# Kernel tuning notes

Measured on AMD Instinct MI355X. Metric: run time of the kernel, lower is better.

## Reference

```python
import jax, jax.numpy as jnp
import numpy as np
import math

B, T, J, D = 16, 243, 24, 256
H, W = 8, 4  # num_heads, half-window


def setup_inputs() -> dict:
    key = jax.random.key(0)
    k1, k2 = jax.random.split(key, 2)
    x_tan_seq = jax.random.normal(k1, (B, T, J, D), dtype=jnp.float32)
    W_qkv = jax.random.normal(k2, (3 * D, D), dtype=jnp.float32) * 0.02
    b_qkv = jnp.zeros((3 * D,), dtype=jnp.float32)
    tau = jnp.ones((H,), dtype=jnp.float32)
    return {"x_tan_seq": x_tan_seq, "W_qkv": W_qkv, "b_qkv": b_qkv, "tau": tau}


def reference(x_tan_seq, W_qkv, b_qkv, tau):
    Bb, Tt, Jj, Dd = x_tan_seq.shape
    d_h = Dd // H
    KW = 2 * W + 1
    # [B,T,J,D] -> [B*J, T, D]
    x = x_tan_seq.transpose(0, 2, 1, 3).reshape(Bb * Jj, Tt, Dd)
    # fused qkv projection (torch Linear: x @ W.T + b)
    qkv = x @ W_qkv.T + b_qkv                      # [BJ, T, 3D]
    qkv = qkv.reshape(Bb * Jj, Tt, 3, H, d_h)
    q = qkv[:, :, 0].transpose(0, 2, 1, 3)          # [BJ, H, T, dh]
    k = qkv[:, :, 1].transpose(0, 2, 1, 3)
    v = qkv[:, :, 2].transpose(0, 2, 1, 3)
    # replicate-pad time axis, then gather sliding windows
    k_pad = jnp.pad(k, ((0, 0), (0, 0), (W, W), (0, 0)), mode='edge')
    v_pad = jnp.pad(v, ((0, 0), (0, 0), (W, W), (0, 0)), mode='edge')
    idx = jnp.arange(Tt)[:, None] + jnp.arange(KW)[None, :]  # [T, KW] into padded axis
    k_win = k_pad[:, :, idx, :]                    # [BJ, H, T, KW, dh]
    v_win = v_pad[:, :, idx, :]
    tau_c = jnp.clip(tau, 0.001)[None, :, None, None]  # clamp(min=0.001)
    logits = jnp.einsum('bhtd,bhtkd->bhtk', q, k_win) / (math.sqrt(d_h) * tau_c)
    # mask out-of-bounds (replicated) frames
    frame = jnp.arange(Tt)[:, None] + (jnp.arange(KW)[None, :] - W)
    oob = (frame < 0) | (frame >= Tt)              # [T, KW]
    logits = jnp.where(oob[None, None], -jnp.inf, logits)
    attn = jax.nn.softmax(logits, axis=-1)
    agg = jnp.einsum('bhtk,bhtkd->bhtd', attn, v_win)  # [BJ, H, T, dh]
    out = agg.transpose(0, 2, 1, 3).reshape(Bb, Jj, Tt, Dd).transpose(0, 2, 1, 3)
    return out  # [B, T, J, D]
```

## Files before the change

### kernel.cpp

```cpp
#include <hip/hip_runtime.h>
#include <hip/hip_bf16.h>
#include <math.h>

typedef __hip_bfloat16 bf16;
typedef __attribute__((ext_vector_type(8))) short short8;
typedef __attribute__((ext_vector_type(4))) float float4v;

#define Tsz 243
#define Jsz 24
#define Dsz 256
#define Hsz 8
#define Wsz 4
#define KWsz 9
#define SEQ 384
#define Ksz 256
#define JDsz 6144
#define MB 128
#define T0B 122

#define XN_ELEMS 23887872
#define XN4 5971968
#define WN4 49152
#define TOT4 (XN4 + WN4)

#define LDST 72
#define KOFFs 5120
#define VTOFFs 10240
#define VTSTR 136
#define POFFs 16128
#define PSTR 72
#define SMEM_SHORTS (POFFs + 8 * 16 * PSTR)
#define SMEM_BYTES (SMEM_SHORTS * 2)

__device__ __forceinline__ bool tau_is_fp32(const void* tau) {
    return *(const unsigned int*)tau == 0x3F800000u;
}

__device__ __forceinline__ unsigned int pack2(float a, float b) {
    const unsigned int lo = (unsigned int)__builtin_bit_cast(unsigned short, __float2bfloat16(a));
    const unsigned int hi = (unsigned int)__builtin_bit_cast(unsigned short, __float2bfloat16(b));
    return lo | (hi << 16);
}
__device__ __forceinline__ unsigned short bf16bits(float x) {
    return __builtin_bit_cast(unsigned short, __float2bfloat16(x));
}

__global__ __launch_bounds__(256, 4)
void conv_prepass(const void* __restrict__ xp, const void* __restrict__ Wp,
                  const void* __restrict__ taup, unsigned int* __restrict__ ws)
{
    if (!tau_is_fp32(taup)) return;
    const float4* xf = (const float4*)xp;
    const float4* wf = (const float4*)Wp;
    const int stride = (int)gridDim.x * 256;
    for (int i = (int)blockIdx.x * 256 + (int)threadIdx.x; i < TOT4; i += stride) {
        const float4 v = (i < XN4) ? xf[i] : wf[i - XN4];
        ((uint2*)ws)[i] = make_uint2(pack2(v.x, v.y), pack2(v.z, v.w));
    }
}

__global__ __launch_bounds__(512, 6)
void fused_qkv_attn(const void* __restrict__ xp, const void* __restrict__ Wp,
                    const void* __restrict__ bp, const void* __restrict__ taup,
                    const bf16* __restrict__ wsb, void* __restrict__ out)
{
    __shared__ __align__(16) bf16 smem[SMEM_SHORTS];
    bf16* As = smem;
    bf16* Bs = smem + 128 * LDST;
    unsigned short* s16 = (unsigned short*)smem;

    const bool is32 = tau_is_fp32(taup);
    const bf16* xAll = is32 ? wsb : (const bf16*)xp;
    const bf16* wAll = is32 ? (wsb + XN_ELEMS) : (const bf16*)Wp;

    const int bid     = (int)blockIdx.x;
    const int logical = (bid & 7) * (SEQ * Hsz * 2 / 8) + (bid >> 3);
    const int s    = logical >> 4;
    const int h    = (logical >> 1) & 7;
    const int blk2 = logical & 1;
    const int b = s / Jsz;
    const int j = s - b * Jsz;
    const int r0 = blk2 ? (Tsz - MB) : 0;

    const int tid  = (int)threadIdx.x;
    const int wave = tid >> 6;
    const int lane = tid & 63;
    const int fr = lane & 15;
    const int fk = (lane >> 4) * 8;
    const int wm32 = (wave >> 1) * 32;
    const int wn   = (wave & 1) * 48;

    const int arow = tid >> 2;
    const int acol = (tid & 3) << 4;
    const bf16* xw = xAll + ((size_t)(b * Tsz + r0 + arow) * Jsz + j) * (size_t)Dsz + acol;
    bf16* aDst = As + arow * LDST + acol;

    const int brow = tid >> 2;
    const int bcol = (tid & 3) << 4;
    const int wrow = ((brow >> 5) << 8) + (h << 5) + (brow & 31);
    const bf16* ww = wAll + (size_t)wrow * Ksz + bcol;
    bf16* bDst = Bs + brow * LDST + bcol;

    float4v acc[2][3];
#pragma unroll
    for (int i = 0; i < 2; ++i)
#pragma unroll
        for (int n = 0; n < 3; ++n)
            acc[i][n] = (float4v){0.f, 0.f, 0.f, 0.f};

    for (int kt = 0; kt < Ksz; kt += 64) {
        {
            const uint4 a0 = *(const uint4*)(xw + kt);
            const uint4 a1 = *(const uint4*)(xw + kt + 8);
            *(uint4*)aDst       = a0;
            *(uint4*)(aDst + 8) = a1;
            if (tid < 384) {
                const uint4 b0 = *(const uint4*)(ww + kt);
                const uint4 b1 = *(const uint4*)(ww + kt + 8);
                *(uint4*)bDst       = b0;
                *(uint4*)(bDst + 8) = b1;
            }
        }
        __syncthreads();
#pragma unroll
        for (int ks = 0; ks < 2; ++ks) {
            short8 af[2], bfr[3];
#pragma unroll
            for (int i = 0; i < 2; ++i)
                af[i] = *(const short8*)(As + (wm32 + (i << 4) + fr) * LDST + (ks << 5) + fk);
#pragma unroll
            for (int n = 0; n < 3; ++n)
                bfr[n] = *(const short8*)(Bs + (wn + (n << 4) + fr) * LDST + (ks << 5) + fk);
#pragma unroll
            for (int i = 0; i < 2; ++i)
#pragma unroll
                for (int n = 0; n < 3; ++n)
                    acc[i][n] = __builtin_amdgcn_mfma_f32_16x16x32_bf16(af[i], bfr[n], acc[i][n], 0, 0, 0);
        }
        __syncthreads();
    }

    const int r0acc = (lane >> 4) << 2;
    if ((wave & 1) == 0) {
        const float b0 = is32 ? ((const float*)bp)[(h << 5) + fr]        : __bfloat162float(((const bf16*)bp)[(h << 5) + fr]);
        const float b1 = is32 ? ((const float*)bp)[(h << 5) + 16 + fr]   : __bfloat162float(((const bf16*)bp)[(h << 5) + 16 + fr]);
        const float b2 = is32 ? ((const float*)bp)[256 + (h << 5) + fr]  : __bfloat162float(((const bf16*)bp)[256 + (h << 5) + fr]);
#pragma unroll
        for (int i = 0; i < 2; ++i) {
            const int tb = wm32 + (i << 4) + r0acc;
#pragma unroll
            for (int r = 0; r < 4; ++r) {
                const int t = tb + r;
                s16[t * 40 + fr]              = bf16bits(acc[i][0][r] + b0);
                s16[t * 40 + 16 + fr]         = bf16bits(acc[i][1][r] + b1);
                s16[KOFFs + t * 40 + fr]      = bf16bits(acc[i][2][r] + b2);
            }
        }
    } else {
        const float b0 = is32 ? ((const float*)bp)[256 + (h << 5) + 16 + fr] : __bfloat162float(((const bf16*)bp)[256 + (h << 5) + 16 + fr]);
        const float b1 = is32 ? ((const float*)bp)[512 + (h << 5) + fr]      : __bfloat162float(((const bf16*)bp)[512 + (h << 5) + fr]);
        const float b2 = is32 ? ((const float*)bp)[512 + (h << 5) + 16 + fr] : __bfloat162float(((const bf16*)bp)[512 + (h << 5) + 16 + fr]);
#pragma unroll
        for (int i = 0; i < 2; ++i) {
            const int tb = wm32 + (i << 4) + r0acc;
#pragma unroll
            for (int r = 0; r < 4; ++r) {
                const int t = tb + r;
                s16[KOFFs + t * 40 + 16 + fr]        = bf16bits(acc[i][0][r] + b0);
                s16[VTOFFs + fr * VTSTR + t]         = bf16bits(acc[i][1][r] + b1);
                s16[VTOFFs + (16 + fr) * VTSTR + t]  = bf16bits(acc[i][2][r] + b2);
            }
        }
    }
    __syncthreads();

    const float tv = is32 ? ((const float*)taup)[h]
                          : __bfloat162float(((const bf16*)taup)[h]);
    const float scale = 1.0f / (5.656854249f * fmaxf(tv, 0.001f));
    const int g  = wave;
    const int wb = (g <= 1) ? 0 : ((g >= 5) ? 64 : ((g - 1) << 4));

    const short8 qf = *(const short8*)((const bf16*)s16 + (g * 16 + fr) * 40 + fk);
    float4v sacc[4];
#pragma unroll
    for (int s2 = 0; s2 < 4; ++s2) {
        const short8 kf = *(const short8*)((const bf16*)s16 + KOFFs + (wb + s2 * 16 + fr) * 40 + fk);
        sacc[s2] = __builtin_amdgcn_mfma_f32_16x16x32_bf16(qf, kf, (float4v){0.f,0.f,0.f,0.f}, 0, 0, 0);
    }

    float vv[4][4];
    const int dly = (lane & 15) + wb - (g << 4) - r0acc;
#pragma unroll
    for (int s2 = 0; s2 < 4; ++s2)
#pragma unroll
        for (int r = 0; r < 4; ++r) {
            const int dd = dly + s2 * 16 - r;
            vv[s2][r] = ((unsigned)(dd + 4) <= 8u) ? sacc[s2][r] * scale : -1e30f;
        }

    float inv[4];
#pragma unroll
    for (int r = 0; r < 4; ++r) {
        float m = fmaxf(fmaxf(vv[0][r], vv[1][r]), fmaxf(vv[2][r], vv[3][r]));
        m = fmaxf(m, __shfl_xor(m, 1, 64));
        m = fmaxf(m, __shfl_xor(m, 2, 64));
        m = fmaxf(m, __shfl_xor(m, 4, 64));
        m = fmaxf(m, __shfl_xor(m, 8, 64));
        float dsum = 0.f;
#pragma unroll
        for (int s2 = 0; s2 < 4; ++s2) {
            vv[s2][r] = __expf(vv[s2][r] - m);
            dsum += vv[s2][r];
        }
        dsum += __shfl_xor(dsum, 1, 64);
        dsum += __shfl_xor(dsum, 2, 64);
        dsum += __shfl_xor(dsum, 4, 64);
        dsum += __shfl_xor(dsum, 8, 64);
        inv[r] = 1.0f / fmaxf(dsum, 1e-30f);
    }

    unsigned short* pb = s16 + POFFs + g * (16 * PSTR);
#pragma unroll
    for (int s2 = 0; s2 < 4; ++s2)
#pragma unroll
        for (int r = 0; r < 4; ++r)
            pb[(r0acc + r) * PSTR + s2 * 16 + (lane & 15)] = bf16bits(vv[s2][r] * inv[r]);

    float4v oacc[2] = {(float4v){0.f,0.f,0.f,0.f}, (float4v){0.f,0.f,0.f,0.f}};
#pragma unroll
    for (int ks = 0; ks < 2; ++ks) {
        const short8 pa = *(const short8*)((const bf16*)pb + fr * PSTR + ks * 32 + fk);
#pragma unroll
        for (int nt = 0; nt < 2; ++nt) {
            const short8 vb = *(const short8*)((const bf16*)s16 + VTOFFs +
                                               (nt * 16 + fr) * VTSTR + wb + ks * 32 + fk);
            oacc[nt] = __builtin_amdgcn_mfma_f32_16x16x32_bf16(pa, vb, oacc[nt], 0, 0, 0);
        }
    }

#pragma unroll
    for (int r = 0; r < 4; ++r) {
        const int tl   = (g << 4) + r0acc + r;
        const int tOut = r0 + tl;
        const bool own = blk2 ? (tOut >= T0B) : (tOut < T0B);
        if (own) {
            const size_t obase = ((size_t)(b * Tsz + tOut) * Jsz + j) * (size_t)Dsz
                               + (h << 5) + (lane & 15);
            if (is32) {
                ((float*)out)[obase]      = oacc[0][r];
                ((float*)out)[obase + 16] = oacc[1][r];
            } else {
                ((bf16*)out)[obase]      = __float2bfloat16(oacc[0][r]);
                ((bf16*)out)[obase + 16] = __float2bfloat16(oacc[1][r]);
            }
        }
    }
}

extern "C" void kernel_launch(void* const* d_in, const int* in_sizes, int n_in,
                              void* d_out, int out_size, void* d_ws, size_t ws_size,
                              hipStream_t stream) {
    (void)in_sizes; (void)n_in; (void)out_size; (void)ws_size;
    conv_prepass<<<2048, 256, 0, stream>>>(d_in[0], d_in[1], d_in[3], (unsigned int*)d_ws);
    fused_qkv_attn<<<SEQ * Hsz * 2, 512, 0, stream>>>(d_in[0], d_in[1], d_in[2], d_in[3],
                                                      (const bf16*)d_ws, d_out);
}
```

Baseline: 255.0 us.

## Transpose x to sequence-major in prepass and shrink attention window tiles

The prepass now writes x into [B,J,T,D] order, so the fused kernel's A-tile loads read contiguous rows instead of rows strided by J*D. The attention stage now uses a 32-key window per 16-query group instead of 64, which halves the QK and PV MFMAs, the softmax work and the P buffer size. The prepass also runs in the bf16 path and uses twice as many blocks. The cost is the index divisions in the prepass and scattered writes to the workspace.

```diff
diff --git a/kernel.cpp b/kernel.cpp
--- a/kernel.cpp
+++ b/kernel.cpp
@@ -11,26 +11,21 @@
 #define Dsz 256
 #define Hsz 8
 #define Wsz 4
-#define KWsz 9
 #define SEQ 384
 #define Ksz 256
-#define JDsz 6144
 #define MB 128
 #define T0B 122
 
 #define XN_ELEMS 23887872
-#define XN4 5971968
-#define WN4 49152
-#define TOT4 (XN4 + WN4)
+#define XU2 5971968
+#define WU2 49152
 
 #define LDST 72
 #define KOFFs 5120
 #define VTOFFs 10240
 #define VTSTR 136
 #define POFFs 16128
-#define PSTR 72
-#define SMEM_SHORTS (POFFs + 8 * 16 * PSTR)
-#define SMEM_BYTES (SMEM_SHORTS * 2)
+#define SMEM_SHORTS (POFFs + 8 * 16 * 40)
 
 __device__ __forceinline__ bool tau_is_fp32(const void* tau) {
     return *(const unsigned int*)tau == 0x3F800000u;
@@ -47,21 +42,38 @@
 
 __global__ __launch_bounds__(256, 4)
 void conv_prepass(const void* __restrict__ xp, const void* __restrict__ Wp,
-                  const void* __restrict__ taup, unsigned int* __restrict__ ws)
+                  const void* __restrict__ taup, uint2* __restrict__ ws)
 {
-    if (!tau_is_fp32(taup)) return;
-    const float4* xf = (const float4*)xp;
-    const float4* wf = (const float4*)Wp;
+    const bool is32 = tau_is_fp32(taup);
     const int stride = (int)gridDim.x * 256;
-    for (int i = (int)blockIdx.x * 256 + (int)threadIdx.x; i < TOT4; i += stride) {
-        const float4 v = (i < XN4) ? xf[i] : wf[i - XN4];
-        ((uint2*)ws)[i] = make_uint2(pack2(v.x, v.y), pack2(v.z, v.w));
+    const int tid0 = (int)blockIdx.x * 256 + (int)threadIdx.x;
+    for (int i = tid0; i < XU2; i += stride) {
+        const int d4 = i & 63;
+        const int r  = i >> 6;
+        const int jj = r % Jsz;
+        const int r2 = r / Jsz;
+        const int t  = r2 % Tsz;
+        const int bb = r2 / Tsz;
+        const int o  = ((bb * Jsz + jj) * Tsz + t) * 64 + d4;
+        if (is32) {
+            const float4 v = ((const float4*)xp)[i];
+            ws[o] = make_uint2(pack2(v.x, v.y), pack2(v.z, v.w));
+        } else {
+            ws[o] = ((const uint2*)xp)[i];
+        }
+    }
+    for (int i = tid0; i < WU2; i += stride) {
+        if (is32) {
+            const float4 v = ((const float4*)Wp)[i];
+            ws[XU2 + i] = make_uint2(pack2(v.x, v.y), pack2(v.z, v.w));
+        } else {
+            ws[XU2 + i] = ((const uint2*)Wp)[i];
+        }
     }
 }
 
 __global__ __launch_bounds__(512, 6)
-void fused_qkv_attn(const void* __restrict__ xp, const void* __restrict__ Wp,
-                    const void* __restrict__ bp, const void* __restrict__ taup,
+void fused_qkv_attn(const void* __restrict__ bp, const void* __restrict__ taup,
                     const bf16* __restrict__ wsb, void* __restrict__ out)
 {
     __shared__ __align__(16) bf16 smem[SMEM_SHORTS];
@@ -70,8 +82,8 @@
     unsigned short* s16 = (unsigned short*)smem;
 
     const bool is32 = tau_is_fp32(taup);
-    const bf16* xAll = is32 ? wsb : (const bf16*)xp;
-    const bf16* wAll = is32 ? (wsb + XN_ELEMS) : (const bf16*)Wp;
+    const bf16* xAll = wsb;
+    const bf16* wAll = wsb + XN_ELEMS;
 
     const int bid     = (int)blockIdx.x;
     const int logical = (bid & 7) * (SEQ * Hsz * 2 / 8) + (bid >> 3);
@@ -92,7 +104,7 @@
 
     const int arow = tid >> 2;
     const int acol = (tid & 3) << 4;
-    const bf16* xw = xAll + ((size_t)(b * Tsz + r0 + arow) * Jsz + j) * (size_t)Dsz + acol;
+    const bf16* xw = xAll + ((size_t)(s * Tsz + r0 + arow)) * (size_t)Dsz + acol;
     bf16* aDst = As + arow * LDST + acol;
 
     const int brow = tid >> 2;
@@ -142,18 +154,18 @@
 
     const int r0acc = (lane >> 4) << 2;
     if ((wave & 1) == 0) {
-        const float b0 = is32 ? ((const float*)bp)[(h << 5) + fr]        : __bfloat162float(((const bf16*)bp)[(h << 5) + fr]);
-        const float b1 = is32 ? ((const float*)bp)[(h << 5) + 16 + fr]   : __bfloat162float(((const bf16*)bp)[(h << 5) + 16 + fr]);
-        const float b2 = is32 ? ((const float*)bp)[256 + (h << 5) + fr]  : __bfloat162float(((const bf16*)bp)[256 + (h << 5) + fr]);
+        const float b0 = is32 ? ((const float*)bp)[(h << 5) + fr]       : __bfloat162float(((const bf16*)bp)[(h << 5) + fr]);
+        const float b1 = is32 ? ((const float*)bp)[(h << 5) + 16 + fr]  : __bfloat162float(((const bf16*)bp)[(h << 5) + 16 + fr]);
+        const float b2 = is32 ? ((const float*)bp)[256 + (h << 5) + fr] : __bfloat162float(((const bf16*)bp)[256 + (h << 5) + fr]);
 #pragma unroll
         for (int i = 0; i < 2; ++i) {
             const int tb = wm32 + (i << 4) + r0acc;
 #pragma unroll
             for (int r = 0; r < 4; ++r) {
                 const int t = tb + r;
-                s16[t * 40 + fr]              = bf16bits(acc[i][0][r] + b0);
-                s16[t * 40 + 16 + fr]         = bf16bits(acc[i][1][r] + b1);
-                s16[KOFFs + t * 40 + fr]      = bf16bits(acc[i][2][r] + b2);
+                s16[t * 40 + fr]         = bf16bits(acc[i][0][r] + b0);
+                s16[t * 40 + 16 + fr]    = bf16bits(acc[i][1][r] + b1);
+                s16[KOFFs + t * 40 + fr] = bf16bits(acc[i][2][r] + b2);
             }
         }
     } else {
@@ -166,9 +178,9 @@
 #pragma unroll
             for (int r = 0; r < 4; ++r) {
                 const int t = tb + r;
-                s16[KOFFs + t * 40 + 16 + fr]        = bf16bits(acc[i][0][r] + b0);
-                s16[VTOFFs + fr * VTSTR + t]         = bf16bits(acc[i][1][r] + b1);
-                s16[VTOFFs + (16 + fr) * VTSTR + t]  = bf16bits(acc[i][2][r] + b2);
+                s16[KOFFs + t * 40 + 16 + fr]       = bf16bits(acc[i][0][r] + b0);
+                s16[VTOFFs + fr * VTSTR + t]        = bf16bits(acc[i][1][r] + b1);
+                s16[VTOFFs + (16 + fr) * VTSTR + t] = bf16bits(acc[i][2][r] + b2);
             }
         }
     }
@@ -177,21 +189,22 @@
     const float tv = is32 ? ((const float*)taup)[h]
                           : __bfloat162float(((const bf16*)taup)[h]);
     const float scale = 1.0f / (5.656854249f * fmaxf(tv, 0.001f));
-    const int g  = wave;
-    const int wb = (g <= 1) ? 0 : ((g >= 5) ? 64 : ((g - 1) << 4));
+    const int g = wave;
+    int wb2 = (g << 4) - 8;
+    wb2 = wb2 < 0 ? 0 : (wb2 > 96 ? 96 : wb2);
 
     const short8 qf = *(const short8*)((const bf16*)s16 + (g * 16 + fr) * 40 + fk);
-    float4v sacc[4];
-#pragma unroll
-    for (int s2 = 0; s2 < 4; ++s2) {
-        const short8 kf = *(const short8*)((const bf16*)s16 + KOFFs + (wb + s2 * 16 + fr) * 40 + fk);
+    float4v sacc[2];
+#pragma unroll
+    for (int s2 = 0; s2 < 2; ++s2) {
+        const short8 kf = *(const short8*)((const bf16*)s16 + KOFFs + (wb2 + s2 * 16 + fr) * 40 + fk);
         sacc[s2] = __builtin_amdgcn_mfma_f32_16x16x32_bf16(qf, kf, (float4v){0.f,0.f,0.f,0.f}, 0, 0, 0);
     }
 
-    float vv[4][4];
-    const int dly = (lane & 15) + wb - (g << 4) - r0acc;
-#pragma unroll
-    for (int s2 = 0; s2 < 4; ++s2)
+    float vv[2][4];
+    const int dly = (lane & 15) + wb2 - (g << 4) - r0acc;
+#pragma unroll
+    for (int s2 = 0; s2 < 2; ++s2)
 #pragma unroll
         for (int r = 0; r < 4; ++r) {
             const int dd = dly + s2 * 16 - r;
@@ -201,17 +214,14 @@
     float inv[4];
 #pragma unroll
     for (int r = 0; r < 4; ++r) {
-        float m = fmaxf(fmaxf(vv[0][r], vv[1][r]), fmaxf(vv[2][r], vv[3][r]));
+        float m = fmaxf(vv[0][r], vv[1][r]);
         m = fmaxf(m, __shfl_xor(m, 1, 64));
         m = fmaxf(m, __shfl_xor(m, 2, 64));
         m = fmaxf(m, __shfl_xor(m, 4, 64));
         m = fmaxf(m, __shfl_xor(m, 8, 64));
-        float dsum = 0.f;
-#pragma unroll
-        for (int s2 = 0; s2 < 4; ++s2) {
-            vv[s2][r] = __expf(vv[s2][r] - m);
-            dsum += vv[s2][r];
-        }
+        vv[0][r] = __expf(vv[0][r] - m);
+        vv[1][r] = __expf(vv[1][r] - m);
+        float dsum = vv[0][r] + vv[1][r];
         dsum += __shfl_xor(dsum, 1, 64);
         dsum += __shfl_xor(dsum, 2, 64);
         dsum += __shfl_xor(dsum, 4, 64);
@@ -219,23 +229,20 @@
         inv[r] = 1.0f / fmaxf(dsum, 1e-30f);
     }
 
-    unsigned short* pb = s16 + POFFs + g * (16 * PSTR);
-#pragma unroll
-    for (int s2 = 0; s2 < 4; ++s2)
+    unsigned short* pb = s16 + POFFs + g * (16 * 40);
+#pragma unroll
+    for (int s2 = 0; s2 < 2; ++s2)
 #pragma unroll
         for (int r = 0; r < 4; ++r)
-            pb[(r0acc + r) * PSTR + s2 * 16 + (lane & 15)] = bf16bits(vv[s2][r] * inv[r]);
-
-    float4v oacc[2] = {(float4v){0.f,0.f,0.f,0.f}, (float4v){0.f,0.f,0.f,0.f}};
-#pragma unroll
-    for (int ks = 0; ks < 2; ++ks) {
-        const short8 pa = *(const short8*)((const bf16*)pb + fr * PSTR + ks * 32 + fk);
-#pragma unroll
-        for (int nt = 0; nt < 2; ++nt) {
-            const short8 vb = *(const short8*)((const bf16*)s16 + VTOFFs +
-                                               (nt * 16 + fr) * VTSTR + wb + ks * 32 + fk);
-            oacc[nt] = __builtin_amdgcn_mfma_f32_16x16x32_bf16(pa, vb, oacc[nt], 0, 0, 0);
-        }
+            pb[(r0acc + r) * 40 + s2 * 16 + (lane & 15)] = bf16bits(vv[s2][r] * inv[r]);
+
+    const short8 pa = *(const short8*)((const bf16*)pb + fr * 40 + fk);
+    float4v oacc[2];
+#pragma unroll
+    for (int nt = 0; nt < 2; ++nt) {
+        const short8 vb = *(const short8*)((const bf16*)s16 + VTOFFs +
+                                           (nt * 16 + fr) * VTSTR + wb2 + fk);
+        oacc[nt] = __builtin_amdgcn_mfma_f32_16x16x32_bf16(pa, vb, (float4v){0.f,0.f,0.f,0.f}, 0, 0, 0);
     }
 
 #pragma unroll
@@ -261,7 +268,7 @@
                               void* d_out, int out_size, void* d_ws, size_t ws_size,
                               hipStream_t stream) {
     (void)in_sizes; (void)n_in; (void)out_size; (void)ws_size;
-    conv_prepass<<<2048, 256, 0, stream>>>(d_in[0], d_in[1], d_in[3], (unsigned int*)d_ws);
-    fused_qkv_attn<<<SEQ * Hsz * 2, 512, 0, stream>>>(d_in[0], d_in[1], d_in[2], d_in[3],
+    conv_prepass<<<4096, 256, 0, stream>>>(d_in[0], d_in[1], d_in[3], (uint2*)d_ws);
+    fused_qkv_attn<<<SEQ * Hsz * 2, 512, 0, stream>>>(d_in[2], d_in[3],
                                                       (const bf16*)d_ws, d_out);
 }
```

Result: faster. 249.1 us (-2.3%).
